# Performance work log

Measured on AMD Instinct MI355X. Metric: run time of the kernel, lower is better.

The kernel has to match this reference:

```python
import jax, jax.numpy as jnp
import numpy as np

B, L, D, H, FFN = 4, 1024, 1024, 16, 4096
DPH = D // H
EPS = 1e-5

def layer_norm(x, g, b):
    mu = jnp.mean(x, axis=-1, keepdims=True)
    var = jnp.mean(jnp.square(x - mu), axis=-1, keepdims=True)
    return (x - mu) * jax.lax.rsqrt(var + EPS) * g + b

def setup_inputs() -> dict:
    key = jax.random.key(0)
    ks = jax.random.split(key, 12)
    s = 0.02
    return {
        "inputs": jax.random.normal(ks[0], (B, L, D), dtype=jnp.float32),
        "Wq": jax.random.normal(ks[1], (D, D), dtype=jnp.float32) * s,
        "bq": jnp.zeros((D,), jnp.float32),
        "Wk": jax.random.normal(ks[2], (D, D), dtype=jnp.float32) * s,
        "bk": jnp.zeros((D,), jnp.float32),
        "Wv": jax.random.normal(ks[3], (D, D), dtype=jnp.float32) * s,
        "bv": jnp.zeros((D,), jnp.float32),
        "Wo": jax.random.normal(ks[4], (D, D), dtype=jnp.float32) * s,
        "bo": jnp.zeros((D,), jnp.float32),
        "ln1_g": jnp.ones((D,), jnp.float32),
        "ln1_b": jnp.zeros((D,), jnp.float32),
        "W1": jax.random.normal(ks[5], (D, FFN), dtype=jnp.float32) * s,  # conv1d k=1 == linear
        "b1": jnp.zeros((FFN,), jnp.float32),
        "W2": jax.random.normal(ks[6], (FFN, D), dtype=jnp.float32) * s,
        "b2": jnp.zeros((D,), jnp.float32),
        "ln2_g": jnp.ones((D,), jnp.float32),
        "ln2_b": jnp.zeros((D,), jnp.float32),
    }

def reference(inputs, Wq, bq, Wk, bk, Wv, bv, Wo, bo, ln1_g, ln1_b,
              W1, b1, W2, b2, ln2_g, ln2_b):
    residual = inputs
    # QKV projections, then the original's raw view(B*H, L, DPH) split (NOT a transpose split)
    q = (inputs @ Wq + bq).reshape(B * H, L, DPH)
    k = (inputs @ Wk + bk).reshape(B * H, L, DPH)
    v = (inputs @ Wv + bv).reshape(B * H, L, DPH)
    scale = DPH ** -0.5
    scores = jnp.einsum('bqd,bkd->bqk', q, k) * scale  # [B*H, L, L]
    attention = jax.nn.softmax(scores, axis=-1)
    context = jnp.einsum('bqk,bkd->bqd', attention, v).reshape(B, L, D)
    out = context @ Wo + bo
    out = layer_norm(residual + out, ln1_g, ln1_b)
    # Positionwise FFN: two 1x1 conv1d == two linears with relu
    ffn = jax.nn.relu(out @ W1 + b1) @ W2 + b2
    out = layer_norm(out + ffn, ln2_g, ln2_b)
    return out, attention
```

## Files before the change

### kernel.cpp

```cpp
#include <hip/hip_runtime.h>
#include <hip/hip_bf16.h>
#include <stdint.h>


using bf16_t  = __hip_bfloat16;
using short8  = __attribute__((ext_vector_type(8))) short;
using short4v = __attribute__((ext_vector_type(4))) short;
using f32x4   = __attribute__((ext_vector_type(4))) float;

#define DEV static __device__ __forceinline__

DEV short bfbits(float f) {
  bf16_t h = __float2bfloat16(f);
  union { bf16_t h; short s; } u; u.h = h; return u.s;
}

DEV void gload_lds16(const bf16_t* g, bf16_t* lds) {
  __builtin_amdgcn_global_load_lds(
      (const __attribute__((address_space(1))) void*)g,
      (__attribute__((address_space(3))) void*)lds, 16, 0, 0);
}

__global__ __launch_bounds__(256) void k_f32_to_bf16(const float* __restrict__ in,
                                                     bf16_t* __restrict__ out) {
  size_t i = ((size_t)blockIdx.x * 256 + threadIdx.x) * 4;
  f32x4 x = *(const f32x4*)(in + i);
  short4v o;
  o[0] = bfbits(x[0]); o[1] = bfbits(x[1]); o[2] = bfbits(x[2]); o[3] = bfbits(x[3]);
  *(short4v*)((short*)out + i) = o;
}

__global__ __launch_bounds__(256) void k_transpose_f32_bf16(const float* __restrict__ in,
                                                            bf16_t* __restrict__ out,
                                                            int R, int C) {
  __shared__ float tile[32][33];
  int tx = threadIdx.x & 31, ty = threadIdx.x >> 5;
  int r0 = blockIdx.y * 32, c0 = blockIdx.x * 32;
  #pragma unroll
  for (int i = 0; i < 4; ++i)
    tile[ty + i * 8][tx] = in[(size_t)(r0 + ty + i * 8) * C + c0 + tx];
  __syncthreads();
  #pragma unroll
  for (int i = 0; i < 4; ++i)
    out[(size_t)(c0 + ty + i * 8) * R + r0 + tx] = __float2bfloat16(tile[tx][ty + i * 8]);
}

__global__ __launch_bounds__(256) void k_transpose_bf16_b(const bf16_t* __restrict__ in,
                                                          bf16_t* __restrict__ out,
                                                          int R, int C, long sIn, long sOut) {
  __shared__ bf16_t tile[32][33];
  const bf16_t* inz = in + (size_t)blockIdx.z * sIn;
  bf16_t* outz = out + (size_t)blockIdx.z * sOut;
  int tx = threadIdx.x & 31, ty = threadIdx.x >> 5;
  int r0 = blockIdx.y * 32, c0 = blockIdx.x * 32;
  #pragma unroll
  for (int i = 0; i < 4; ++i)
    tile[ty + i * 8][tx] = inz[(size_t)(r0 + ty + i * 8) * C + c0 + tx];
  __syncthreads();
  #pragma unroll
  for (int i = 0; i < 4; ++i)
    outz[(size_t)(c0 + ty + i * 8) * R + r0 + tx] = tile[tx][ty + i * 8];
}

template<int BM, int BN, bool ALPHA, bool BIAS, bool RELU, bool RESID,
         bool OUTF, bool OUTB, bool QKV3>
__global__ __launch_bounds__(256)
void k_gemm_bt(const bf16_t* __restrict__ A, const bf16_t* __restrict__ Bt,
               float* __restrict__ Cf, bf16_t* __restrict__ Cb,
               const float* __restrict__ bias, const float* __restrict__ bias2,
               const float* __restrict__ bias3, const float* __restrict__ resid,
               int Kdim, int lda, int ldb, int ldc, float alpha) {
  constexpr int BK = 32;
  constexpr int WTM = BM / 2, WTN = BN / 2;
  constexpr int MI = WTM / 16, NI = WTN / 16;
  __shared__ __align__(16) bf16_t sA[BM * BK];
  __shared__ __align__(16) bf16_t sB[BN * BK];

  const int tid = threadIdx.x;
  const int lane = tid & 63;
  const int wv = tid >> 6;
  const int wm = wv & 1, wn = wv >> 1;
  const size_t m0 = (size_t)blockIdx.y * BM;
  const size_t n0 = (size_t)blockIdx.x * BN;

  f32x4 acc[MI][NI] = {};

  const int rr = lane >> 2, cc = (lane & 3) * 8;
  const bf16_t* Arow = A + (m0 + rr) * (size_t)lda + cc;
  const bf16_t* Brow = Bt + (n0 + rr) * (size_t)ldb + cc;

  const int fm = wm * WTM + (lane & 15);
  const int fn = wn * WTN + (lane & 15);
  const int fk = (lane >> 4) * 8;

  for (int k0 = 0; k0 < Kdim; k0 += BK) {
    #pragma unroll
    for (int j = 0; j < BM / 64; ++j) {
      int c = j * 4 + wv;
      gload_lds16(Arow + (size_t)c * 16 * lda + k0, sA + c * 512);
    }
    #pragma unroll
    for (int j = 0; j < BN / 64; ++j) {
      int c = j * 4 + wv;
      gload_lds16(Brow + (size_t)c * 16 * ldb + k0, sB + c * 512);
    }
    __syncthreads();

    short8 av[MI], bvv[NI];
    #pragma unroll
    for (int mi = 0; mi < MI; ++mi) av[mi] = *(const short8*)(sA + (fm + mi * 16) * BK + fk);
    #pragma unroll
    for (int ni = 0; ni < NI; ++ni) bvv[ni] = *(const short8*)(sB + (fn + ni * 16) * BK + fk);
    #pragma unroll
    for (int mi = 0; mi < MI; ++mi)
      #pragma unroll
      for (int ni = 0; ni < NI; ++ni)
        acc[mi][ni] = __builtin_amdgcn_mfma_f32_16x16x32_bf16(av[mi], bvv[ni],
                                                              acc[mi][ni], 0, 0, 0);
    __syncthreads();
  }

  const int tz = QKV3 ? (int)(n0 >> 10) : 0;
  const float* bp = BIAS ? (QKV3 ? (tz == 0 ? bias : (tz == 1 ? bias2 : bias3))
                                 : bias) : nullptr;
  bf16_t* cb = QKV3 ? (Cb + (size_t)tz * 4194304) : Cb;
  const int col0 = (int)n0 + wn * WTN + (lane & 15);
  const int row0 = (int)m0 + wm * WTM + ((lane >> 4) << 2);
  #pragma unroll
  for (int ni = 0; ni < NI; ++ni) {
    const int col = col0 + ni * 16;
    const int colw = QKV3 ? (col & 1023) : col;
    const float bval = BIAS ? bp[colw] : 0.0f;
    #pragma unroll
    for (int mi = 0; mi < MI; ++mi) {
      #pragma unroll
      for (int r = 0; r < 4; ++r) {
        int row = row0 + mi * 16 + r;
        float v = acc[mi][ni][r];
        if (ALPHA) v *= alpha;
        v += bval;
        size_t off = (size_t)row * ldc + colw;
        if (RESID) v += resid[off];
        if (RELU) v = fmaxf(v, 0.0f);
        if (OUTF) Cf[off] = v;
        if (OUTB) cb[off] = __float2bfloat16(v);
      }
    }
  }
}

__global__ __launch_bounds__(256) void k_flash_attn(const bf16_t* __restrict__ Qb,
                                                    const bf16_t* __restrict__ Kb,
                                                    const bf16_t* __restrict__ Vt,
                                                    float* __restrict__ attn,
                                                    bf16_t* __restrict__ ctx) {
  constexpr int LP = 72;
  __shared__ __align__(16) bf16_t sQ[128][LP];
  __shared__ __align__(16) bf16_t sK[64][LP];
  __shared__ __align__(16) bf16_t sP[128][LP];
  __shared__ __align__(16) bf16_t sV[64][LP];

  const int tid = threadIdx.x;
  const int lane = tid & 63;
  const int wv = tid >> 6;
  const int z = blockIdx.y;
  const int m0 = blockIdx.x * 128;

  const bf16_t* Qz = Qb + (size_t)z * 65536;
  const bf16_t* Kz = Kb + (size_t)z * 65536;
  const bf16_t* Vz = Vt + (size_t)z * 65536;
  float* az = attn + (size_t)z * 1048576;
  bf16_t* cz = ctx + (size_t)z * 65536;

  #pragma unroll
  for (int j = 0; j < 4; ++j) {
    int ii = j * 256 + tid;
    int r = ii >> 3, c = (ii & 7) * 8;
    *(short8*)(&sQ[r][c]) = *(const short8*)(Qz + (size_t)(m0 + r) * 64 + c);
  }
  __syncthreads();

  const int fr = lane & 15;
  const int fk = (lane >> 4) * 8;
  const int crow = (lane >> 4) << 2;

  short8 qf[2][2];
  #pragma unroll
  for (int mi = 0; mi < 2; ++mi)
    #pragma unroll
    for (int ks = 0; ks < 2; ++ks)
      qf[mi][ks] = *(const short8*)(&sQ[wv * 32 + mi * 16 + fr][ks * 32 + fk]);

  float m_run[2][4], s_run[2][4];
  #pragma unroll
  for (int mi = 0; mi < 2; ++mi)
    #pragma unroll
    for (int r = 0; r < 4; ++r) { m_run[mi][r] = -1e30f; s_run[mi][r] = 0.0f; }

  for (int c0 = 0; c0 < 1024; c0 += 64) {
    #pragma unroll
    for (int j = 0; j < 2; ++j) {
      int ii = j * 256 + tid;
      int r = ii >> 3, c = (ii & 7) * 8;
      *(short8*)(&sK[r][c]) = *(const short8*)(Kz + (size_t)(c0 + r) * 64 + c);
    }
    __syncthreads();
    f32x4 acc[2][4] = {};
    #pragma unroll
    for (int ks = 0; ks < 2; ++ks) {
      short8 bf[4];
      #pragma unroll
      for (int ni = 0; ni < 4; ++ni)
        bf[ni] = *(const short8*)(&sK[ni * 16 + fr][ks * 32 + fk]);
      #pragma unroll
      for (int mi = 0; mi < 2; ++mi)
        #pragma unroll
        for (int ni = 0; ni < 4; ++ni)
          acc[mi][ni] = __builtin_amdgcn_mfma_f32_16x16x32_bf16(qf[mi][ks], bf[ni],
                                                                acc[mi][ni], 0, 0, 0);
    }
    __syncthreads();
    #pragma unroll
    for (int mi = 0; mi < 2; ++mi)
      #pragma unroll
      for (int r = 0; r < 4; ++r) {
        float mx = acc[mi][0][r];
        #pragma unroll
        for (int ni = 1; ni < 4; ++ni) mx = fmaxf(mx, acc[mi][ni][r]);
        mx *= 0.125f;
        #pragma unroll
        for (int o = 1; o < 16; o <<= 1) mx = fmaxf(mx, __shfl_xor(mx, o, 64));
        float mn = fmaxf(m_run[mi][r], mx);
        float se = 0.0f;
        #pragma unroll
        for (int ni = 0; ni < 4; ++ni) se += __expf(acc[mi][ni][r] * 0.125f - mn);
        #pragma unroll
        for (int o = 1; o < 16; o <<= 1) se += __shfl_xor(se, o, 64);
        s_run[mi][r] = s_run[mi][r] * __expf(m_run[mi][r] - mn) + se;
        m_run[mi][r] = mn;
      }
  }

  float inv_s[2][4];
  #pragma unroll
  for (int mi = 0; mi < 2; ++mi)
    #pragma unroll
    for (int r = 0; r < 4; ++r) inv_s[mi][r] = 1.0f / s_run[mi][r];

  f32x4 cacc[2][4] = {};
  for (int c0 = 0; c0 < 1024; c0 += 64) {
    #pragma unroll
    for (int j = 0; j < 2; ++j) {
      int ii = j * 256 + tid;
      int r = ii >> 3, c = (ii & 7) * 8;
      *(short8*)(&sK[r][c]) = *(const short8*)(Kz + (size_t)(c0 + r) * 64 + c);
      *(short8*)(&sV[r][c]) = *(const short8*)(Vz + (size_t)r * 1024 + c0 + c);
    }
    __syncthreads();
    f32x4 acc[2][4] = {};
    #pragma unroll
    for (int ks = 0; ks < 2; ++ks) {
      short8 bf[4];
      #pragma unroll
      for (int ni = 0; ni < 4; ++ni)
        bf[ni] = *(const short8*)(&sK[ni * 16 + fr][ks * 32 + fk]);
      #pragma unroll
      for (int mi = 0; mi < 2; ++mi)
        #pragma unroll
        for (int ni = 0; ni < 4; ++ni)
          acc[mi][ni] = __builtin_amdgcn_mfma_f32_16x16x32_bf16(qf[mi][ks], bf[ni],
                                                                acc[mi][ni], 0, 0, 0);
    }
    #pragma unroll
    for (int mi = 0; mi < 2; ++mi)
      #pragma unroll
      for (int ni = 0; ni < 4; ++ni)
        #pragma unroll
        for (int r = 0; r < 4; ++r) {
          int row = wv * 32 + mi * 16 + crow + r;
          float p = __expf(acc[mi][ni][r] * 0.125f - m_run[mi][r]) * inv_s[mi][r];
          az[(size_t)(m0 + row) * 1024 + c0 + ni * 16 + fr] = p;
          sP[row][ni * 16 + fr] = __float2bfloat16(p);
        }
    __syncthreads();
    #pragma unroll
    for (int ks = 0; ks < 2; ++ks) {
      short8 pa[2], vb[4];
      #pragma unroll
      for (int mi = 0; mi < 2; ++mi)
        pa[mi] = *(const short8*)(&sP[wv * 32 + mi * 16 + fr][ks * 32 + fk]);
      #pragma unroll
      for (int ni = 0; ni < 4; ++ni)
        vb[ni] = *(const short8*)(&sV[ni * 16 + fr][ks * 32 + fk]);
      #pragma unroll
      for (int mi = 0; mi < 2; ++mi)
        #pragma unroll
        for (int ni = 0; ni < 4; ++ni)
          cacc[mi][ni] = __builtin_amdgcn_mfma_f32_16x16x32_bf16(pa[mi], vb[ni],
                                                                 cacc[mi][ni], 0, 0, 0);
    }
    __syncthreads();
  }

  #pragma unroll
  for (int mi = 0; mi < 2; ++mi)
    #pragma unroll
    for (int ni = 0; ni < 4; ++ni)
      #pragma unroll
      for (int r = 0; r < 4; ++r) {
        int row = wv * 32 + mi * 16 + crow + r;
        cz[(size_t)(m0 + row) * 64 + ni * 16 + fr] = __float2bfloat16(cacc[mi][ni][r]);
      }
}

__global__ __launch_bounds__(256) void k_layernorm(float* __restrict__ io,
                                                   bf16_t* __restrict__ ob,
                                                   const float* __restrict__ g,
                                                   const float* __restrict__ bta) {
  float* r = io + (size_t)blockIdx.x * 1024;
  const int t = threadIdx.x;
  f32x4 x = *(const f32x4*)(r + t * 4);
  float s = x[0] + x[1] + x[2] + x[3];
  float s2 = x[0] * x[0] + x[1] * x[1] + x[2] * x[2] + x[3] * x[3];
  #pragma unroll
  for (int o = 32; o > 0; o >>= 1) { s += __shfl_xor(s, o, 64); s2 += __shfl_xor(s2, o, 64); }
  __shared__ float as[4], as2[4];
  if ((t & 63) == 0) { as[t >> 6] = s; as2[t >> 6] = s2; }
  __syncthreads();
  s = as[0] + as[1] + as[2] + as[3];
  s2 = as2[0] + as2[1] + as2[2] + as2[3];
  float mu = s * (1.0f / 1024.0f);
  float var = s2 * (1.0f / 1024.0f) - mu * mu;
  float rs = rsqrtf(var + 1e-5f);
  f32x4 gg = *(const f32x4*)(g + t * 4);
  f32x4 bb = *(const f32x4*)(bta + t * 4);
  f32x4 y;
  #pragma unroll
  for (int i = 0; i < 4; ++i) y[i] = (x[i] - mu) * rs * gg[i] + bb[i];
  *(f32x4*)(r + t * 4) = y;
  if (ob) {
    short4v o4;
    o4[0] = bfbits(y[0]); o4[1] = bfbits(y[1]); o4[2] = bfbits(y[2]); o4[3] = bfbits(y[3]);
    *(short4v*)((short*)ob + (size_t)blockIdx.x * 1024 + t * 4) = o4;
  }
}

extern "C" void kernel_launch(void* const* d_in, const int* in_sizes, int n_in,
                              void* d_out, int out_size, void* d_ws, size_t ws_size,
                              hipStream_t stream) {
  (void)in_sizes; (void)n_in; (void)out_size;
  const float* inputs = (const float*)d_in[0];
  const float* Wq = (const float*)d_in[1];  const float* bq = (const float*)d_in[2];
  const float* Wk = (const float*)d_in[3];  const float* bk = (const float*)d_in[4];
  const float* Wv = (const float*)d_in[5];  const float* bv = (const float*)d_in[6];
  const float* Wo = (const float*)d_in[7];  const float* bo = (const float*)d_in[8];
  const float* ln1g = (const float*)d_in[9];  const float* ln1b = (const float*)d_in[10];
  const float* W1 = (const float*)d_in[11]; const float* b1 = (const float*)d_in[12];
  const float* W2 = (const float*)d_in[13]; const float* b2 = (const float*)d_in[14];
  const float* ln2g = (const float*)d_in[15]; const float* ln2b = (const float*)d_in[16];

  const size_t MB = 1ull << 20;
  if (ws_size < 96 * MB) return;

  char* ws = (char*)d_ws;
  bf16_t* WQT  = (bf16_t*)(ws + 0 * MB);
  bf16_t* WKT  = (bf16_t*)(ws + 2 * MB);
  bf16_t* WVT  = (bf16_t*)(ws + 4 * MB);
  bf16_t* WOT  = (bf16_t*)(ws + 6 * MB);
  bf16_t* W1T  = (bf16_t*)(ws + 8 * MB);
  bf16_t* W2T  = (bf16_t*)(ws + 16 * MB);
  bf16_t* XB   = (bf16_t*)(ws + 24 * MB);
  bf16_t* QB   = (bf16_t*)(ws + 32 * MB);
  bf16_t* VB   = (bf16_t*)(ws + 48 * MB);
  bf16_t* VT   = (bf16_t*)(ws + 56 * MB);
  bf16_t* KB   = (bf16_t*)(ws + 40 * MB);
  bf16_t* CTX  = (bf16_t*)(ws + 24 * MB);
  float*  OUT1F = (float*)(ws + 40 * MB);
  bf16_t* OUT1B = (bf16_t*)(ws + 32 * MB);
  bf16_t* HB   = (bf16_t*)(ws + 64 * MB);

  float* outF = (float*)d_out;
  float* attn = outF + 4194304;

  k_f32_to_bf16<<<4096, 256, 0, stream>>>(inputs, XB);
  k_transpose_f32_bf16<<<dim3(32, 32), 256, 0, stream>>>(Wq, WQT, 1024, 1024);
  k_transpose_f32_bf16<<<dim3(32, 32), 256, 0, stream>>>(Wk, WKT, 1024, 1024);
  k_transpose_f32_bf16<<<dim3(32, 32), 256, 0, stream>>>(Wv, WVT, 1024, 1024);
  k_transpose_f32_bf16<<<dim3(32, 32), 256, 0, stream>>>(Wo, WOT, 1024, 1024);
  k_transpose_f32_bf16<<<dim3(128, 32), 256, 0, stream>>>(W1, W1T, 1024, 4096);
  k_transpose_f32_bf16<<<dim3(32, 128), 256, 0, stream>>>(W2, W2T, 4096, 1024);

  k_gemm_bt<128, 128, false, true, false, false, false, true, true>
      <<<dim3(24, 32), 256, 0, stream>>>(XB, WQT, nullptr, QB, bq, bk, bv, nullptr,
                                         1024, 1024, 1024, 1024, 1.0f);

  k_transpose_bf16_b<<<dim3(2, 32, 64), 256, 0, stream>>>(VB, VT, 1024, 64, 65536, 65536);

  k_flash_attn<<<dim3(8, 64), 256, 0, stream>>>(QB, KB, VT, attn, CTX);

  k_gemm_bt<128, 128, false, true, false, true, true, false, false>
      <<<dim3(8, 32), 256, 0, stream>>>(CTX, WOT, OUT1F, nullptr, bo, nullptr, nullptr,
                                        inputs, 1024, 1024, 1024, 1024, 1.0f);

  k_layernorm<<<4096, 256, 0, stream>>>(OUT1F, OUT1B, ln1g, ln1b);

  k_gemm_bt<128, 128, false, true, true, false, false, true, false>
      <<<dim3(32, 32), 256, 0, stream>>>(OUT1B, W1T, nullptr, HB, b1, nullptr, nullptr,
                                         nullptr, 1024, 1024, 1024, 4096, 1.0f);

  k_gemm_bt<128, 128, false, true, false, true, true, false, false>
      <<<dim3(8, 32), 256, 0, stream>>>(HB, W2T, outF, nullptr, b2, nullptr, nullptr,
                                        OUT1F, 4096, 4096, 4096, 1024, 1.0f);

  k_layernorm<<<4096, 256, 0, stream>>>(outF, nullptr, ln2g, ln2b);
}
```

Measured before the change: 707.7 us.

## Double-buffer K/V tiles in flash attention with register prefetch, fold scale into Q

The flash-attention kernel now keeps two LDS buffers for K and V. The next tile is prefetched into registers two iterations ahead, so global loads overlap the MFMA and softmax work and one barrier per iteration is removed. The 1/sqrt(d) scale is applied in the QKV GEMM epilogue instead of inside the attention loops. The four square weight transposes are merged into one launch. The sP write/read now relies on an lgkmcnt wait rather than a block barrier, which risks a cross-wave race, since each wave reads only its own rows but LDS visibility across lanes still needs ordering.

```diff
diff --git a/kernel.cpp b/kernel.cpp
--- a/kernel.cpp
+++ b/kernel.cpp
@@ -43,6 +43,26 @@
   #pragma unroll
   for (int i = 0; i < 4; ++i)
     out[(size_t)(c0 + ty + i * 8) * R + r0 + tx] = __float2bfloat16(tile[tx][ty + i * 8]);
+}
+
+__global__ __launch_bounds__(256) void k_transpose4_f32_bf16(
+    const float* __restrict__ w0, const float* __restrict__ w1,
+    const float* __restrict__ w2, const float* __restrict__ w3,
+    bf16_t* __restrict__ o0, bf16_t* __restrict__ o1,
+    bf16_t* __restrict__ o2, bf16_t* __restrict__ o3) {
+  __shared__ float tile[32][33];
+  const int zz = blockIdx.z;
+  const float* in = zz == 0 ? w0 : zz == 1 ? w1 : zz == 2 ? w2 : w3;
+  bf16_t* out = zz == 0 ? o0 : zz == 1 ? o1 : zz == 2 ? o2 : o3;
+  int tx = threadIdx.x & 31, ty = threadIdx.x >> 5;
+  int r0 = blockIdx.y * 32, c0 = blockIdx.x * 32;
+  #pragma unroll
+  for (int i = 0; i < 4; ++i)
+    tile[ty + i * 8][tx] = in[(size_t)(r0 + ty + i * 8) * 1024 + c0 + tx];
+  __syncthreads();
+  #pragma unroll
+  for (int i = 0; i < 4; ++i)
+    out[(size_t)(c0 + ty + i * 8) * 1024 + r0 + tx] = __float2bfloat16(tile[tx][ty + i * 8]);
 }
 
 __global__ __launch_bounds__(256) void k_transpose_bf16_b(const bf16_t* __restrict__ in,
@@ -124,6 +144,7 @@
   const float* bp = BIAS ? (QKV3 ? (tz == 0 ? bias : (tz == 1 ? bias2 : bias3))
                                  : bias) : nullptr;
   bf16_t* cb = QKV3 ? (Cb + (size_t)tz * 4194304) : Cb;
+  const float qscale = (QKV3 && tz == 0) ? 0.125f : 1.0f;
   const int col0 = (int)n0 + wn * WTN + (lane & 15);
   const int row0 = (int)m0 + wm * WTM + ((lane >> 4) << 2);
   #pragma unroll
@@ -139,6 +160,7 @@
         float v = acc[mi][ni][r];
         if (ALPHA) v *= alpha;
         v += bval;
+        if (QKV3) v *= qscale;
         size_t off = (size_t)row * ldc + colw;
         if (RESID) v += resid[off];
         if (RELU) v = fmaxf(v, 0.0f);
@@ -156,9 +178,9 @@
                                                     bf16_t* __restrict__ ctx) {
   constexpr int LP = 72;
   __shared__ __align__(16) bf16_t sQ[128][LP];
-  __shared__ __align__(16) bf16_t sK[64][LP];
+  __shared__ __align__(16) bf16_t sK[2][64][LP];
+  __shared__ __align__(16) bf16_t sV[2][64][LP];
   __shared__ __align__(16) bf16_t sP[128][LP];
-  __shared__ __align__(16) bf16_t sV[64][LP];
 
   const int tid = threadIdx.x;
   const int lane = tid & 63;
@@ -172,12 +194,12 @@
   float* az = attn + (size_t)z * 1048576;
   bf16_t* cz = ctx + (size_t)z * 65536;
 
-  #pragma unroll
-  for (int j = 0; j < 4; ++j) {
-    int ii = j * 256 + tid;
-    int r = ii >> 3, c = (ii & 7) * 8;
-    *(short8*)(&sQ[r][c]) = *(const short8*)(Qz + (size_t)(m0 + r) * 64 + c);
-  }
+  const int sr = tid >> 3, sc = (tid & 7) * 8;
+
+  #pragma unroll
+  for (int j = 0; j < 4; ++j)
+    *(short8*)(&sQ[j * 32 + sr][sc]) =
+        *(const short8*)(Qz + (size_t)(m0 + j * 32 + sr) * 64 + sc);
   __syncthreads();
 
   const int fr = lane & 15;
@@ -197,21 +219,38 @@
     #pragma unroll
     for (int r = 0; r < 4; ++r) { m_run[mi][r] = -1e30f; s_run[mi][r] = 0.0f; }
 
-  for (int c0 = 0; c0 < 1024; c0 += 64) {
-    #pragma unroll
-    for (int j = 0; j < 2; ++j) {
-      int ii = j * 256 + tid;
-      int r = ii >> 3, c = (ii & 7) * 8;
-      *(short8*)(&sK[r][c]) = *(const short8*)(Kz + (size_t)(c0 + r) * 64 + c);
-    }
-    __syncthreads();
+  short8 kreg[2], vreg[2];
+
+  #pragma unroll
+  for (int j = 0; j < 2; ++j)
+    kreg[j] = *(const short8*)(Kz + (size_t)(j * 32 + sr) * 64 + sc);
+  #pragma unroll
+  for (int j = 0; j < 2; ++j)
+    *(short8*)(&sK[0][j * 32 + sr][sc]) = kreg[j];
+  #pragma unroll
+  for (int j = 0; j < 2; ++j)
+    kreg[j] = *(const short8*)(Kz + (size_t)(64 + j * 32 + sr) * 64 + sc);
+  __syncthreads();
+
+  for (int c = 0; c < 16; ++c) {
+    const int cur = c & 1;
+    if (c + 1 < 16) {
+      #pragma unroll
+      for (int j = 0; j < 2; ++j)
+        *(short8*)(&sK[cur ^ 1][j * 32 + sr][sc]) = kreg[j];
+    }
+    if (c + 2 < 16) {
+      #pragma unroll
+      for (int j = 0; j < 2; ++j)
+        kreg[j] = *(const short8*)(Kz + (size_t)((c + 2) * 64 + j * 32 + sr) * 64 + sc);
+    }
     f32x4 acc[2][4] = {};
     #pragma unroll
     for (int ks = 0; ks < 2; ++ks) {
       short8 bf[4];
       #pragma unroll
       for (int ni = 0; ni < 4; ++ni)
-        bf[ni] = *(const short8*)(&sK[ni * 16 + fr][ks * 32 + fk]);
+        bf[ni] = *(const short8*)(&sK[cur][ni * 16 + fr][ks * 32 + fk]);
       #pragma unroll
       for (int mi = 0; mi < 2; ++mi)
         #pragma unroll
@@ -219,7 +258,6 @@
           acc[mi][ni] = __builtin_amdgcn_mfma_f32_16x16x32_bf16(qf[mi][ks], bf[ni],
                                                                 acc[mi][ni], 0, 0, 0);
     }
-    __syncthreads();
     #pragma unroll
     for (int mi = 0; mi < 2; ++mi)
       #pragma unroll
@@ -227,18 +265,18 @@
         float mx = acc[mi][0][r];
         #pragma unroll
         for (int ni = 1; ni < 4; ++ni) mx = fmaxf(mx, acc[mi][ni][r]);
-        mx *= 0.125f;
         #pragma unroll
         for (int o = 1; o < 16; o <<= 1) mx = fmaxf(mx, __shfl_xor(mx, o, 64));
         float mn = fmaxf(m_run[mi][r], mx);
         float se = 0.0f;
         #pragma unroll
-        for (int ni = 0; ni < 4; ++ni) se += __expf(acc[mi][ni][r] * 0.125f - mn);
+        for (int ni = 0; ni < 4; ++ni) se += __expf(acc[mi][ni][r] - mn);
         #pragma unroll
         for (int o = 1; o < 16; o <<= 1) se += __shfl_xor(se, o, 64);
         s_run[mi][r] = s_run[mi][r] * __expf(m_run[mi][r] - mn) + se;
         m_run[mi][r] = mn;
       }
+    __syncthreads();
   }
 
   float inv_s[2][4];
@@ -247,23 +285,48 @@
     #pragma unroll
     for (int r = 0; r < 4; ++r) inv_s[mi][r] = 1.0f / s_run[mi][r];
 
+  #pragma unroll
+  for (int j = 0; j < 2; ++j) {
+    kreg[j] = *(const short8*)(Kz + (size_t)(j * 32 + sr) * 64 + sc);
+    vreg[j] = *(const short8*)(Vz + (size_t)(j * 32 + sr) * 1024 + sc);
+  }
+  #pragma unroll
+  for (int j = 0; j < 2; ++j) {
+    *(short8*)(&sK[0][j * 32 + sr][sc]) = kreg[j];
+    *(short8*)(&sV[0][j * 32 + sr][sc]) = vreg[j];
+  }
+  #pragma unroll
+  for (int j = 0; j < 2; ++j) {
+    kreg[j] = *(const short8*)(Kz + (size_t)(64 + j * 32 + sr) * 64 + sc);
+    vreg[j] = *(const short8*)(Vz + (size_t)(j * 32 + sr) * 1024 + 64 + sc);
+  }
+  __syncthreads();
+
   f32x4 cacc[2][4] = {};
-  for (int c0 = 0; c0 < 1024; c0 += 64) {
-    #pragma unroll
-    for (int j = 0; j < 2; ++j) {
-      int ii = j * 256 + tid;
-      int r = ii >> 3, c = (ii & 7) * 8;
-      *(short8*)(&sK[r][c]) = *(const short8*)(Kz + (size_t)(c0 + r) * 64 + c);
-      *(short8*)(&sV[r][c]) = *(const short8*)(Vz + (size_t)r * 1024 + c0 + c);
-    }
-    __syncthreads();
+  for (int c = 0; c < 16; ++c) {
+    const int cur = c & 1;
+    const int c0 = c * 64;
+    if (c + 1 < 16) {
+      #pragma unroll
+      for (int j = 0; j < 2; ++j) {
+        *(short8*)(&sK[cur ^ 1][j * 32 + sr][sc]) = kreg[j];
+        *(short8*)(&sV[cur ^ 1][j * 32 + sr][sc]) = vreg[j];
+      }
+    }
+    if (c + 2 < 16) {
+      #pragma unroll
+      for (int j = 0; j < 2; ++j) {
+        kreg[j] = *(const short8*)(Kz + (size_t)((c + 2) * 64 + j * 32 + sr) * 64 + sc);
+        vreg[j] = *(const short8*)(Vz + (size_t)(j * 32 + sr) * 1024 + (c + 2) * 64 + sc);
+      }
+    }
     f32x4 acc[2][4] = {};
     #pragma unroll
     for (int ks = 0; ks < 2; ++ks) {
       short8 bf[4];
       #pragma unroll
       for (int ni = 0; ni < 4; ++ni)
-        bf[ni] = *(const short8*)(&sK[ni * 16 + fr][ks * 32 + fk]);
+        bf[ni] = *(const short8*)(&sK[cur][ni * 16 + fr][ks * 32 + fk]);
       #pragma unroll
       for (int mi = 0; mi < 2; ++mi)
         #pragma unroll
@@ -278,11 +341,12 @@
         #pragma unroll
         for (int r = 0; r < 4; ++r) {
           int row = wv * 32 + mi * 16 + crow + r;
-          float p = __expf(acc[mi][ni][r] * 0.125f - m_run[mi][r]) * inv_s[mi][r];
+          float p = __expf(acc[mi][ni][r] - m_run[mi][r]) * inv_s[mi][r];
           az[(size_t)(m0 + row) * 1024 + c0 + ni * 16 + fr] = p;
           sP[row][ni * 16 + fr] = __float2bfloat16(p);
         }
-    __syncthreads();
+    asm volatile("s_waitcnt lgkmcnt(0)" ::: "memory");
+    __builtin_amdgcn_sched_barrier(0);
     #pragma unroll
     for (int ks = 0; ks < 2; ++ks) {
       short8 pa[2], vb[4];
@@ -291,7 +355,7 @@
         pa[mi] = *(const short8*)(&sP[wv * 32 + mi * 16 + fr][ks * 32 + fk]);
       #pragma unroll
       for (int ni = 0; ni < 4; ++ni)
-        vb[ni] = *(const short8*)(&sV[ni * 16 + fr][ks * 32 + fk]);
+        vb[ni] = *(const short8*)(&sV[cur][ni * 16 + fr][ks * 32 + fk]);
       #pragma unroll
       for (int mi = 0; mi < 2; ++mi)
         #pragma unroll
@@ -371,9 +435,9 @@
   bf16_t* W2T  = (bf16_t*)(ws + 16 * MB);
   bf16_t* XB   = (bf16_t*)(ws + 24 * MB);
   bf16_t* QB   = (bf16_t*)(ws + 32 * MB);
+  bf16_t* KB   = (bf16_t*)(ws + 40 * MB);
   bf16_t* VB   = (bf16_t*)(ws + 48 * MB);
   bf16_t* VT   = (bf16_t*)(ws + 56 * MB);
-  bf16_t* KB   = (bf16_t*)(ws + 40 * MB);
   bf16_t* CTX  = (bf16_t*)(ws + 24 * MB);
   float*  OUT1F = (float*)(ws + 40 * MB);
   bf16_t* OUT1B = (bf16_t*)(ws + 32 * MB);
@@ -383,10 +447,8 @@
   float* attn = outF + 4194304;
 
   k_f32_to_bf16<<<4096, 256, 0, stream>>>(inputs, XB);
-  k_transpose_f32_bf16<<<dim3(32, 32), 256, 0, stream>>>(Wq, WQT, 1024, 1024);
-  k_transpose_f32_bf16<<<dim3(32, 32), 256, 0, stream>>>(Wk, WKT, 1024, 1024);
-  k_transpose_f32_bf16<<<dim3(32, 32), 256, 0, stream>>>(Wv, WVT, 1024, 1024);
-  k_transpose_f32_bf16<<<dim3(32, 32), 256, 0, stream>>>(Wo, WOT, 1024, 1024);
+  k_transpose4_f32_bf16<<<dim3(32, 32, 4), 256, 0, stream>>>(Wq, Wk, Wv, Wo,
+                                                             WQT, WKT, WVT, WOT);
   k_transpose_f32_bf16<<<dim3(128, 32), 256, 0, stream>>>(W1, W1T, 1024, 4096);
   k_transpose_f32_bf16<<<dim3(32, 128), 256, 0, stream>>>(W2, W2T, 4096, 1024);
 
```

Result: no change. 694.1 us (-1.9%).
